# Optimization experiments

Hardware: AMD Instinct MI355X
Metric: run time of the kernel (lower is better)

The kernel has to match this reference:

```python
import jax, jax.numpy as jnp
import numpy as np
from math import factorial, sqrt

L_MAX = 3
MUL = 64
# e3nn FullyConnectedTensorProduct instruction order: lexicographic over (l1, l2, l3)
# keeping paths with triangle inequality and matching parity ((-1)^(l1+l2) == (-1)^l3).
PATHS = [(l1, l2, l3)
         for l1 in range(L_MAX + 1)
         for l2 in range(L_MAX + 1)
         for l3 in range(L_MAX + 1)
         if abs(l1 - l2) <= l3 <= l1 + l2 and (l1 + l2 + l3) % 2 == 0]
assert len(PATHS) == 23
N_TO = {l3: sum(1 for p in PATHS if p[2] == l3) for l3 in range(L_MAX + 1)}


def _su2_cg(j1, m1, j2, m2, j3, m3):
    # Complex-basis Clebsch-Gordan coefficient (Racah formula), as in e3nn.
    if m3 != m1 + m2:
        return 0.0
    f = factorial
    vmin = max(-j1 + j2 + m3, -j1 + m1, 0)
    vmax = min(j2 + j3 + m1, j3 - j1 + j2, j3 + m3)
    c = sqrt((2 * j3 + 1) * f(j3 + j1 - j2) * f(j3 - j1 + j2) * f(j1 + j2 - j3)
             * f(j3 + m3) * f(j3 - m3)
             / (f(j1 + j2 + j3 + 1) * f(j1 - m1) * f(j1 + m1) * f(j2 - m2) * f(j2 + m2)))
    s = 0.0
    for v in range(vmin, vmax + 1):
        s += (-1) ** (v + j2 + m2) / f(v) * f(j2 + j3 + m1 - v) * f(j1 - m1 + v) \
             / f(j3 - j1 + j2 - v) / f(j3 + m3 - v) / f(v + j1 - j2 - m3)
    return c * s


def _q(l):
    # Change of basis real -> complex spherical harmonics (e3nn convention).
    q = np.zeros((2 * l + 1, 2 * l + 1), dtype=np.complex128)
    for m in range(-l, 0):
        q[l + m, l + abs(m)] = 1.0 / np.sqrt(2.0)
        q[l + m, l - abs(m)] = -1j / np.sqrt(2.0)
    q[l, l] = 1.0
    for m in range(1, l + 1):
        q[l + m, l + abs(m)] = (-1) ** m / np.sqrt(2.0)
        q[l + m, l - abs(m)] = 1j * (-1) ** m / np.sqrt(2.0)
    return (-1j) ** l * q


def _w3j(l1, l2, l3):
    # Real-basis Wigner 3j tensor, unit Frobenius norm (e3nn's o3.wigner_3j).
    csu2 = np.zeros((2 * l1 + 1, 2 * l2 + 1, 2 * l3 + 1))
    for m1 in range(-l1, l1 + 1):
        for m2 in range(-l2, l2 + 1):
            m3 = m1 + m2
            if -l3 <= m3 <= l3:
                csu2[l1 + m1, l2 + m2, l3 + m3] = _su2_cg(l1, m1, l2, m2, l3, m3)
    q1, q2, q3 = _q(l1), _q(l2), _q(l3)
    c = np.einsum('ij,kl,mn,ikn->jlm', q1, q2, np.conj(q3.T), csu2.astype(np.complex128))
    c = np.real(c)
    return (c / np.linalg.norm(c)).astype(np.float32)


W3J = {p: jnp.asarray(_w3j(*p)) for p in PATHS}
# e3nn 'component' irrep_normalization + 'element' path_normalization:
# per-path coeff = sqrt(ir_out.dim / (n_paths_into_out * mul1 * mul2)).
COEFF = {p: float(np.sqrt((2 * p[2] + 1) / (N_TO[p[2]] * MUL * MUL))) for p in PATHS}


def setup_inputs():
    key = jax.random.key(0)
    kx, kw = jax.random.split(key)
    x = jax.random.normal(kx, (2, 1024, MUL * (L_MAX + 1) ** 2), dtype=jnp.float32)
    weights = jax.random.normal(kw, (len(PATHS), MUL, MUL, MUL), dtype=jnp.float32)
    return {"x": x, "weights": weights}


def reference(x, weights):
    B, N, D = x.shape
    Z = B * N
    xf = x.reshape(Z, D)
    # e3nn layout: blocks of (mul, 2l+1) concatenated over l; offset = MUL * l^2.
    xs = [xf[:, MUL * l * l: MUL * (l + 1) ** 2].reshape(Z, MUL, 2 * l + 1)
          for l in range(L_MAX + 1)]
    acc = [jnp.zeros((Z, MUL, 2 * l + 1), dtype=x.dtype) for l in range(L_MAX + 1)]
    for p, (l1, l2, l3) in enumerate(PATHS):
        c = W3J[(l1, l2, l3)]
        t1 = jnp.einsum('zui,ijk->zujk', xs[l1], c)            # [Z,u,2l2+1,2l3+1]
        t2 = jnp.einsum('zujk,zvj->zuvk', t1, xs[l2])          # [Z,u,v,2l3+1]
        seg = jnp.einsum('zuvk,uvw->zwk', t2, weights[p]) * COEFF[(l1, l2, l3)]
        acc[l3] = acc[l3] + seg
    out = jnp.concatenate([a.reshape(Z, -1) for a in acc], axis=-1)
    return out.reshape(B, N, -1)
```

## Files before the change

kernel.cpp:

```cpp
#include <hip/hip_runtime.h>

struct CD { double re, im; };
constexpr CD cmul(CD a, CD b){ return CD{a.re*b.re - a.im*b.im, a.re*b.im + a.im*b.re}; }
constexpr CD conj_(CD a){ return CD{a.re, -a.im}; }

constexpr double factd(int n){ double r = 1.0; for(int i = 2; i <= n; ++i) r *= (double)i; return r; }
constexpr double csqrt_(double x){
  if (x <= 0.0) return 0.0;
  double g = x > 1.0 ? x : 1.0;
  for (int i = 0; i < 100; ++i) g = 0.5*(g + x/g);
  return g;
}

constexpr double su2_cg(int j1,int m1,int j2,int m2,int j3,int m3){
  if (m3 != m1 + m2) return 0.0;
  int vmin = -j1 + j2 + m3;
  if (-j1 + m1 > vmin) vmin = -j1 + m1;
  if (0 > vmin) vmin = 0;
  int vmax = j2 + j3 + m1;
  if (j3 - j1 + j2 < vmax) vmax = j3 - j1 + j2;
  if (j3 + m3 < vmax) vmax = j3 + m3;
  double c = csqrt_((2.0*j3 + 1.0) * factd(j3 + j1 - j2) * factd(j3 - j1 + j2) * factd(j1 + j2 - j3)
                    * factd(j3 + m3) * factd(j3 - m3)
                    / (factd(j1 + j2 + j3 + 1) * factd(j1 - m1) * factd(j1 + m1)
                       * factd(j2 - m2) * factd(j2 + m2)));
  double s = 0.0;
  for (int v = vmin; v <= vmax; ++v){
    double t = (((v + j2 + m2) & 1) ? -1.0 : 1.0) / factd(v)
               * factd(j2 + j3 + m1 - v) * factd(j1 - m1 + v)
               / factd(j3 - j1 + j2 - v) / factd(j3 + m3 - v) / factd(v + j1 - j2 - m3);
    s += t;
  }
  return c * s;
}

struct QM { CD m[7][7]; };
constexpr QM qmat(int l){
  QM q{};
  double is2 = 1.0 / csqrt_(2.0);
  for (int mm = -l; mm < 0; ++mm){
    q.m[l+mm][l-mm] = CD{is2, 0.0};
    q.m[l+mm][l+mm] = CD{0.0, -is2};
  }
  q.m[l][l] = CD{1.0, 0.0};
  for (int mm = 1; mm <= l; ++mm){
    double sgn = (mm & 1) ? -1.0 : 1.0;
    q.m[l+mm][l+mm] = CD{sgn*is2, 0.0};
    q.m[l+mm][l-mm] = CD{0.0, sgn*is2};
  }
  CD ph = (l % 4 == 0) ? CD{1,0} : (l % 4 == 1) ? CD{0,-1} : (l % 4 == 2) ? CD{-1,0} : CD{0,1};
  for (int r = 0; r < 7; ++r)
    for (int c = 0; c < 7; ++c)
      q.m[r][c] = cmul(ph, q.m[r][c]);
  return q;
}

template<int L1,int L2,int L3> struct W3JT { float v[2*L1+1][2*L2+1][2*L3+1]; };

template<int L1,int L2,int L3>
constexpr W3JT<L1,L2,L3> make_w3j(){
  constexpr int D1 = 2*L1+1, D2 = 2*L2+1, D3 = 2*L3+1;
  QM q1 = qmat(L1), q2 = qmat(L2), q3 = qmat(L3);
  double cg[7][7] = {};
  for (int i = 0; i < D1; ++i)
    for (int k = 0; k < D2; ++k){
      int n = i + k - L1 - L2 + L3;
      if (n >= 0 && n < D3) cg[i][k] = su2_cg(L1, i-L1, L2, k-L2, L3, (i-L1)+(k-L2));
    }
  double c[D1][D2][D3] = {};
  double norm2 = 0.0;
  for (int j = 0; j < D1; ++j)
    for (int l = 0; l < D2; ++l)
      for (int m = 0; m < D3; ++m){
        CD s{0.0, 0.0};
        for (int i = 0; i < D1; ++i)
          for (int k = 0; k < D2; ++k){
            double g = cg[i][k];
            if (g == 0.0) continue;
            int n = i + k - L1 - L2 + L3;
            CD t = cmul(q1.m[i][j], q2.m[k][l]);
            t = cmul(t, conj_(q3.m[n][m]));
            s.re += t.re * g; s.im += t.im * g;
          }
        c[j][l][m] = s.re;
        norm2 += s.re * s.re;
      }
  double inv = 1.0 / csqrt_(norm2);
  W3JT<L1,L2,L3> w{};
  for (int j = 0; j < D1; ++j)
    for (int l = 0; l < D2; ++l)
      for (int m = 0; m < D3; ++m){
        double val = c[j][l][m] * inv;
        if (val < 1e-10 && val > -1e-10) val = 0.0;
        w.v[j][l][m] = (float)val;
      }
  return w;
}

__device__ __constant__ int L3P_[23]  = {0,1,2,3,1,0,2,1,3,2,2,1,3,0,2,1,3,3,2,1,3,0,2};
__device__ __constant__ int SWAPP_[23] = {0,1,1,1,0,0,0,1,1,1,0,0,0,0,0,1,1,0,0,0,0,0,0};
constexpr int K3CUM[24] = {0,1,4,9,16,19,20,25,28,35,40,45,48,55,56,61,64,71,78,83,86,93,94,99};
constexpr size_t ZW = 2048ull * 64ull;

typedef __bf16 bf16x8 __attribute__((ext_vector_type(8)));
typedef float  f32x4  __attribute__((ext_vector_type(4)));

__global__ void pack_w_kernel(const float* __restrict__ w, unsigned short* __restrict__ wp, int total){
  int idx = blockIdx.x * 256 + threadIdx.x;
  if (idx >= total) return;
  int e    = idx & 7;
  int lane = (idx >> 3) & 63;
  int nt   = (idx >> 9) & 3;
  int hf   = (idx >> 11) & 1;
  int s    = (idx >> 12) & 63;
  int p    = idx >> 18;
  int kv = hf*32 + (lane >> 4)*8 + e;
  int wc = nt*16 + (lane & 15);
  int l3 = L3P_[p];
  const float nto[4] = {4.f, 6.f, 7.f, 6.f};
  float coeff = sqrtf((2.f*l3 + 1.f) / (nto[l3] * 4096.f));
  int a = SWAPP_[p] ? kv : s;
  int b = SWAPP_[p] ? s : kv;
  float val = w[(((size_t)p*64 + a)*64 + b)*64 + wc] * coeff;
  unsigned bits = __builtin_bit_cast(unsigned, val);
  unsigned r = (bits + 0x7FFFu + ((bits >> 16) & 1u)) >> 16;
  wp[idx] = (unsigned short)r;
}

__global__ void transpose_x(const float* __restrict__ x, float* __restrict__ xT){
  __shared__ float t[32][33];
  int bx = blockIdx.x, by = blockIdx.y;
  int tx = threadIdx.x & 31, ty = threadIdx.x >> 5;
  #pragma unroll
  for (int r = 0; r < 4; ++r)
    t[ty + r*8][tx] = x[(size_t)(by*32 + ty + r*8)*1024 + bx*32 + tx];
  __syncthreads();
  #pragma unroll
  for (int r = 0; r < 4; ++r)
    xT[(size_t)(bx*32 + ty + r*8)*2048 + by*32 + tx] = t[tx][ty + r*8];
}

template<int P,int L1,int L2,int L3,bool SWAP,int G0,int G,bool PART>
__device__ __forceinline__ void run_slot(
    int tile, const float* __restrict__ xT,
    const unsigned short* __restrict__ wp,
    float* __restrict__ dst, float* red)
{
  constexpr int K3 = 2*L3+1;
  constexpr int LK = SWAP ? L1 : L2;
  constexpr int LS = SWAP ? L2 : L1;
  constexpr int DK = 2*LK+1, DS = 2*LS+1;
  constexpr auto C = make_w3j<L1,L2,L3>();

  const int lane = threadIdx.x & 63;
  const int wv   = threadIdx.x >> 6;
  const int zc   = tile*16 + (lane & 15);

  float xk[8][DK];
  {
    const float* xkb = xT + (size_t)(64*LK*LK)*2048 + zc;
    const int t0 = wv*32 + (lane >> 4)*8;
    #pragma unroll
    for (int e = 0; e < 8; ++e)
      #pragma unroll
      for (int t = 0; t < DK; ++t)
        xk[e][t] = xkb[(size_t)((t0 + e)*DK + t)*2048];
  }

  const float* xsb = xT + (size_t)(64*LS*LS)*2048 + zc;
  const unsigned short* wu = wp + (size_t)P*262144 + (size_t)wv*2048 + (size_t)lane*8;

  f32x4 acc[G][4];
  #pragma unroll
  for (int a = 0; a < G; ++a)
    #pragma unroll
    for (int b = 0; b < 4; ++b) acc[a][b] = f32x4{0.f,0.f,0.f,0.f};

  const float* xsp = xsb;
  float xs[DS];
  #pragma unroll
  for (int j = 0; j < DS; ++j) xs[j] = xsp[(size_t)j*2048];

  for (int s = 0; s < 64; ++s){
    bf16x8 bfrag[4];
    #pragma unroll
    for (int nt = 0; nt < 4; ++nt)
      bfrag[nt] = *reinterpret_cast<const bf16x8*>(wu + nt*512);

    const float* xnp = (s < 63) ? xsp + (size_t)DS*2048 : xsp;
    float xn[DS];
    #pragma unroll
    for (int j = 0; j < DS; ++j) xn[j] = xnp[(size_t)j*2048];

    #pragma unroll
    for (int kk = 0; kk < G; ++kk){
      float dk[DK];
      #pragma unroll
      for (int t = 0; t < DK; ++t) dk[t] = 0.f;
      #pragma unroll
      for (int t = 0; t < DK; ++t){
        #pragma unroll
        for (int j = 0; j < DS; ++j){
          const float cv = SWAP ? C.v[t][j][G0+kk] : C.v[j][t][G0+kk];
          if (cv != 0.0f) dk[t] = __builtin_fmaf(xs[j], cv, dk[t]);
        }
      }
      bf16x8 af;
      #pragma unroll
      for (int e = 0; e < 8; ++e){
        float t2 = 0.f;
        #pragma unroll
        for (int t = 0; t < DK; ++t) t2 = __builtin_fmaf(xk[e][t], dk[t], t2);
        af[e] = (__bf16)t2;
      }
      __builtin_amdgcn_s_setprio(1);
      #pragma unroll
      for (int nt = 0; nt < 4; ++nt)
        acc[kk][nt] = __builtin_amdgcn_mfma_f32_16x16x32_bf16(af, bfrag[nt], acc[kk][nt], 0, 0, 0);
      __builtin_amdgcn_s_setprio(0);
    }
    #pragma unroll
    for (int j = 0; j < DS; ++j) xs[j] = xn[j];
    xsp += (size_t)DS*2048;
    wu  += 4096;
  }

  constexpr int Gh = (G + 1) / 2;
  static_assert(Gh <= 3, "red[] sized for Gh<=3");
  auto store_one = [&](int kk, int nt, const f32x4& o, const f32x4& a){
    #pragma unroll
    for (int r = 0; r < 4; ++r){
      int zl = ((lane >> 4) << 2) + r;
      int wc = nt*16 + (lane & 15);
      float val = a[r] + o[r];
      if constexpr (PART){
        dst[(size_t)K3CUM[P]*ZW + (size_t)(tile*16 + zl)*(64*K3) + wc*K3 + (G0+kk)] = val;
      } else {
        unsafeAtomicAdd(dst + (size_t)(tile*16 + zl)*1024 + 64*L3*L3 + wc*K3 + (G0+kk), val);
      }
    }
  };

  if (wv == 1){
    #pragma unroll
    for (int kk = 0; kk < Gh; ++kk)
      #pragma unroll
      for (int nt = 0; nt < 4; ++nt)
        *reinterpret_cast<f32x4*>(&red[((kk*4 + nt)*64 + lane)*4]) = acc[kk][nt];
  }
  __syncthreads();
  if (wv == 0){
    #pragma unroll
    for (int kk = 0; kk < Gh; ++kk)
      #pragma unroll
      for (int nt = 0; nt < 4; ++nt){
        f32x4 o = *reinterpret_cast<const f32x4*>(&red[((kk*4 + nt)*64 + lane)*4]);
        store_one(kk, nt, o, acc[kk][nt]);
      }
  }
  if constexpr (G > Gh){
    if (wv == 0){
      #pragma unroll
      for (int kk = Gh; kk < G; ++kk)
        #pragma unroll
        for (int nt = 0; nt < 4; ++nt)
          *reinterpret_cast<f32x4*>(&red[(((kk-Gh)*4 + nt)*64 + lane)*4]) = acc[kk][nt];
    }
    __syncthreads();
    if (wv == 1){
      #pragma unroll
      for (int kk = Gh; kk < G; ++kk)
        #pragma unroll
        for (int nt = 0; nt < 4; ++nt){
          f32x4 o = *reinterpret_cast<const f32x4*>(&red[(((kk-Gh)*4 + nt)*64 + lane)*4]);
          store_one(kk, nt, o, acc[kk][nt]);
        }
    }
  }
}

template<bool PART>
__global__ __launch_bounds__(128, 3) void tp_main(const float* __restrict__ xT,
    const unsigned short* __restrict__ wp, float* __restrict__ dst)
{
  __shared__ __align__(16) float red[3072];
  const int slot = blockIdx.x >> 7;
  const int tile = blockIdx.x & 127;
  switch (slot){
    case 0:  run_slot< 6,1,1,2,false,0,5,PART>(tile,xT,wp,dst,red); break;
    case 1:  run_slot<16,2,3,3,true ,0,3,PART>(tile,xT,wp,dst,red); break;
    case 2:  run_slot<20,3,2,3,false,0,3,PART>(tile,xT,wp,dst,red); break;
    case 3:  run_slot<14,2,2,2,false,0,3,PART>(tile,xT,wp,dst,red); break;
    case 4:  run_slot<15,2,3,1,true ,0,3,PART>(tile,xT,wp,dst,red); break;
    case 5:  run_slot<19,3,2,1,false,0,3,PART>(tile,xT,wp,dst,red); break;
    case 6:  run_slot< 8,1,2,3,true ,0,4,PART>(tile,xT,wp,dst,red); break;
    case 7:  run_slot<12,2,1,3,false,0,4,PART>(tile,xT,wp,dst,red); break;
    case 8:  run_slot<22,3,3,2,false,0,2,PART>(tile,xT,wp,dst,red); break;
    case 9:  run_slot<22,3,3,2,false,2,2,PART>(tile,xT,wp,dst,red); break;
    case 10: run_slot< 9,1,3,2,true ,0,3,PART>(tile,xT,wp,dst,red); break;
    case 11: run_slot<16,2,3,3,true ,3,2,PART>(tile,xT,wp,dst,red); break;
    case 12: run_slot<16,2,3,3,true ,5,2,PART>(tile,xT,wp,dst,red); break;
    case 13: run_slot<20,3,2,3,false,3,2,PART>(tile,xT,wp,dst,red); break;
    case 14: run_slot<20,3,2,3,false,5,2,PART>(tile,xT,wp,dst,red); break;
    case 15: run_slot< 2,0,2,2,true ,0,5,PART>(tile,xT,wp,dst,red); break;
    case 16: run_slot<10,2,0,2,false,0,5,PART>(tile,xT,wp,dst,red); break;
    case 17: run_slot<11,2,1,1,false,0,3,PART>(tile,xT,wp,dst,red); break;
    case 18: run_slot< 7,1,2,1,true ,0,3,PART>(tile,xT,wp,dst,red); break;
    case 19: run_slot<18,3,1,2,false,0,3,PART>(tile,xT,wp,dst,red); break;
    case 20: run_slot< 8,1,2,3,true ,4,3,PART>(tile,xT,wp,dst,red); break;
    case 21: run_slot<12,2,1,3,false,4,3,PART>(tile,xT,wp,dst,red); break;
    case 22: run_slot<14,2,2,2,false,3,2,PART>(tile,xT,wp,dst,red); break;
    case 23: run_slot< 9,1,3,2,true ,3,2,PART>(tile,xT,wp,dst,red); break;
    case 24: run_slot<18,3,1,2,false,3,2,PART>(tile,xT,wp,dst,red); break;
    case 25: run_slot<22,3,3,2,false,4,1,PART>(tile,xT,wp,dst,red); break;
    case 26: run_slot<21,3,3,0,false,0,1,PART>(tile,xT,wp,dst,red); break;
    case 27: run_slot< 3,0,3,3,true ,0,4,PART>(tile,xT,wp,dst,red); break;
    case 28: run_slot<17,3,0,3,false,0,4,PART>(tile,xT,wp,dst,red); break;
    case 29: run_slot< 3,0,3,3,true ,4,3,PART>(tile,xT,wp,dst,red); break;
    case 30: run_slot<17,3,0,3,false,4,3,PART>(tile,xT,wp,dst,red); break;
    case 31: run_slot< 1,0,1,1,true ,0,3,PART>(tile,xT,wp,dst,red); break;
    case 32: run_slot< 4,1,0,1,false,0,3,PART>(tile,xT,wp,dst,red); break;
    case 33: run_slot<13,2,2,0,false,0,1,PART>(tile,xT,wp,dst,red); break;
    case 34: run_slot< 5,1,1,0,false,0,1,PART>(tile,xT,wp,dst,red); break;
    case 35: run_slot< 0,0,0,0,false,0,1,PART>(tile,xT,wp,dst,red); break;
    default: break;
  }
}

__global__ void gather_out(const float* __restrict__ part, float* __restrict__ out){
  int gid = blockIdx.x * 256 + threadIdx.x;
  int z = gid >> 10, j = gid & 1023;
  float s;
  if (j < 64){
    size_t b = (size_t)z*64 + j;
    s = part[(size_t)K3CUM[0]*ZW + b] + part[(size_t)K3CUM[5]*ZW + b]
      + part[(size_t)K3CUM[13]*ZW + b] + part[(size_t)K3CUM[21]*ZW + b];
  } else if (j < 256){
    size_t b = (size_t)z*192 + (j - 64);
    s = part[(size_t)K3CUM[1]*ZW + b] + part[(size_t)K3CUM[4]*ZW + b]
      + part[(size_t)K3CUM[7]*ZW + b] + part[(size_t)K3CUM[11]*ZW + b]
      + part[(size_t)K3CUM[15]*ZW + b] + part[(size_t)K3CUM[19]*ZW + b];
  } else if (j < 576){
    size_t b = (size_t)z*320 + (j - 256);
    s = part[(size_t)K3CUM[2]*ZW + b] + part[(size_t)K3CUM[6]*ZW + b]
      + part[(size_t)K3CUM[9]*ZW + b] + part[(size_t)K3CUM[10]*ZW + b]
      + part[(size_t)K3CUM[14]*ZW + b] + part[(size_t)K3CUM[18]*ZW + b]
      + part[(size_t)K3CUM[22]*ZW + b];
  } else {
    size_t b = (size_t)z*448 + (j - 576);
    s = part[(size_t)K3CUM[3]*ZW + b] + part[(size_t)K3CUM[8]*ZW + b]
      + part[(size_t)K3CUM[12]*ZW + b] + part[(size_t)K3CUM[16]*ZW + b]
      + part[(size_t)K3CUM[17]*ZW + b] + part[(size_t)K3CUM[20]*ZW + b];
  }
  out[gid] = s;
}

extern "C" void kernel_launch(void* const* d_in, const int* in_sizes, int n_in,
                              void* d_out, int out_size, void* d_ws, size_t ws_size,
                              hipStream_t stream)
{
  const float* x = (const float*)d_in[0];
  const float* w = (const float*)d_in[1];
  float* out = (float*)d_out;

  const size_t packB = 23ull*64*2*4*64*8 * sizeof(unsigned short);
  const size_t xTB   = 1024ull*2048*sizeof(float);
  const size_t partB = 99ull*ZW*sizeof(float);
  const int totalW = 23*64*2*4*64*8;

  unsigned short* wp = (unsigned short*)d_ws;
  float* xT   = (float*)((char*)d_ws + packB);
  float* part = (float*)((char*)d_ws + packB + xTB);

  if (ws_size < packB + xTB) return;

  pack_w_kernel<<<(totalW + 255)/256, 256, 0, stream>>>(w, wp, totalW);
  dim3 tg(32, 64);
  transpose_x<<<tg, 256, 0, stream>>>(x, xT);

  if (ws_size >= packB + xTB + partB){
    tp_main<true><<<36*128, 128, 0, stream>>>(xT, wp, part);
    gather_out<<<(2048*1024)/256, 256, 0, stream>>>(part, out);
  } else {
    hipMemsetAsync(d_out, 0, (size_t)out_size * sizeof(float), stream);
    tp_main<false><<<36*128, 128, 0, stream>>>(xT, wp, out);
  }
}
```

Before: 206.1 us.

## Pack four z-tiles per 512-thread block and pipeline the wave-pair reduction in phases

Each block now has 512 threads, organised as four wave pairs that each handle their own 16-row z tile, so the grid shrinks fourfold. The aim is for co-resident waves to share weight-fragment loads through cache and to cut per-block launch overhead. The cross-wave reduction becomes a loop of two-slice phases that alternate which wave writes, using a per-pair LDS region. This adds block-wide barriers across all four pairs, raises LDS use to 32 KB, and changes launch bounds to 512 threads with 2 blocks per CU, which may reduce occupancy or raise register pressure.

```diff
diff --git a/kernel.cpp b/kernel.cpp
--- a/kernel.cpp
+++ b/kernel.cpp
@@ -153,8 +153,11 @@
   constexpr auto C = make_w3j<L1,L2,L3>();
 
   const int lane = threadIdx.x & 63;
-  const int wv   = threadIdx.x >> 6;
-  const int zc   = tile*16 + (lane & 15);
+  const int wid  = threadIdx.x >> 6;
+  const int wv   = wid & 1;
+  const int pr   = wid >> 1;
+  const int zc   = tile*64 + pr*16 + (lane & 15);
+  float* redp = red + pr*2048;
 
   float xk[8][DK];
   {
@@ -225,8 +228,6 @@
     wu  += 4096;
   }
 
-  constexpr int Gh = (G + 1) / 2;
-  static_assert(Gh <= 3, "red[] sized for Gh<=3");
   auto store_one = [&](int kk, int nt, const f32x4& o, const f32x4& a){
     #pragma unroll
     for (int r = 0; r < 4; ++r){
@@ -234,58 +235,45 @@
       int wc = nt*16 + (lane & 15);
       float val = a[r] + o[r];
       if constexpr (PART){
-        dst[(size_t)K3CUM[P]*ZW + (size_t)(tile*16 + zl)*(64*K3) + wc*K3 + (G0+kk)] = val;
+        dst[(size_t)K3CUM[P]*ZW + (size_t)(tile*64 + pr*16 + zl)*(64*K3) + wc*K3 + (G0+kk)] = val;
       } else {
-        unsafeAtomicAdd(dst + (size_t)(tile*16 + zl)*1024 + 64*L3*L3 + wc*K3 + (G0+kk), val);
+        unsafeAtomicAdd(dst + (size_t)(tile*64 + pr*16 + zl)*1024 + 64*L3*L3 + wc*K3 + (G0+kk), val);
       }
     }
   };
 
-  if (wv == 1){
-    #pragma unroll
-    for (int kk = 0; kk < Gh; ++kk)
-      #pragma unroll
-      for (int nt = 0; nt < 4; ++nt)
-        *reinterpret_cast<f32x4*>(&red[((kk*4 + nt)*64 + lane)*4]) = acc[kk][nt];
-  }
-  __syncthreads();
-  if (wv == 0){
-    #pragma unroll
-    for (int kk = 0; kk < Gh; ++kk)
-      #pragma unroll
-      for (int nt = 0; nt < 4; ++nt){
-        f32x4 o = *reinterpret_cast<const f32x4*>(&red[((kk*4 + nt)*64 + lane)*4]);
-        store_one(kk, nt, o, acc[kk][nt]);
-      }
-  }
-  if constexpr (G > Gh){
-    if (wv == 0){
-      #pragma unroll
-      for (int kk = Gh; kk < G; ++kk)
+  constexpr int NPH = (G + 1) / 2;
+  #pragma unroll
+  for (int ph = 0; ph < NPH; ++ph){
+    const int base = 2*ph;
+    const int cnt  = (G - base) < 2 ? (G - base) : 2;
+    const int writer = ph & 1;
+    if (wv == writer){
+      for (int q = 0; q < cnt; ++q)
         #pragma unroll
         for (int nt = 0; nt < 4; ++nt)
-          *reinterpret_cast<f32x4*>(&red[(((kk-Gh)*4 + nt)*64 + lane)*4]) = acc[kk][nt];
+          *reinterpret_cast<f32x4*>(&redp[((q*4 + nt)*64 + lane)*4]) = acc[base+q][nt];
     }
     __syncthreads();
-    if (wv == 1){
-      #pragma unroll
-      for (int kk = Gh; kk < G; ++kk)
+    if (wv != writer){
+      for (int q = 0; q < cnt; ++q)
         #pragma unroll
         for (int nt = 0; nt < 4; ++nt){
-          f32x4 o = *reinterpret_cast<const f32x4*>(&red[(((kk-Gh)*4 + nt)*64 + lane)*4]);
-          store_one(kk, nt, o, acc[kk][nt]);
+          f32x4 o = *reinterpret_cast<const f32x4*>(&redp[((q*4 + nt)*64 + lane)*4]);
+          store_one(base+q, nt, o, acc[base+q][nt]);
         }
     }
+    if (ph + 1 < NPH) __syncthreads();
   }
 }
 
 template<bool PART>
-__global__ __launch_bounds__(128, 3) void tp_main(const float* __restrict__ xT,
+__global__ __launch_bounds__(512, 2) void tp_main(const float* __restrict__ xT,
     const unsigned short* __restrict__ wp, float* __restrict__ dst)
 {
-  __shared__ __align__(16) float red[3072];
-  const int slot = blockIdx.x >> 7;
-  const int tile = blockIdx.x & 127;
+  __shared__ __align__(16) float red[8192];
+  const int slot = blockIdx.x >> 5;
+  const int tile = blockIdx.x & 31;
   switch (slot){
     case 0:  run_slot< 6,1,1,2,false,0,5,PART>(tile,xT,wp,dst,red); break;
     case 1:  run_slot<16,2,3,3,true ,0,3,PART>(tile,xT,wp,dst,red); break;
@@ -379,10 +367,10 @@
   transpose_x<<<tg, 256, 0, stream>>>(x, xT);
 
   if (ws_size >= packB + xTB + partB){
-    tp_main<true><<<36*128, 128, 0, stream>>>(xT, wp, part);
+    tp_main<true><<<36*32, 512, 0, stream>>>(xT, wp, part);
     gather_out<<<(2048*1024)/256, 256, 0, stream>>>(part, out);
   } else {
     hipMemsetAsync(d_out, 0, (size_t)out_size * sizeof(float), stream);
-    tp_main<false><<<36*128, 128, 0, stream>>>(xT, wp, out);
-  }
-}
+    tp_main<false><<<36*32, 512, 0, stream>>>(xT, wp, out);
+  }
+}
```

Measured after the change: 211.2 us. 2.4% more time.
